# Kernel optimization log

Measured on AMD Instinct MI355X. Metric: run time of the kernel, lower is better.

## Reference

```python
import jax, jax.numpy as jnp
import numpy as np

L = 4          # n_layers
A = 4          # aspect heads: causal, intentional, temporal, normative
D = 1024       # d_model
DK = D // A    # 256
S = 3072
NE, NA = 1536, 1024  # n_events, n_agents (norms = S - NE - NA)
EPS = 1e-5


def _layernorm(x, g, b):
    mu = jnp.mean(x, axis=-1, keepdims=True)
    var = jnp.mean(jnp.square(x - mu), axis=-1, keepdims=True)
    return g * (x - mu) * jax.lax.rsqrt(var + EPS) + b


def setup_inputs() -> dict:
    key = jax.random.key(0)
    ks = jax.random.split(key, 12)
    s = 0.02
    return {
        "hidden": jax.random.normal(ks[0], (1, S, D), jnp.float32),
        "Wq": jax.random.normal(ks[1], (L, D, D), jnp.float32) * s,
        "bq": jnp.zeros((L, D), jnp.float32),
        "Wk": jax.random.normal(ks[2], (L, D, D), jnp.float32) * s,
        "bk": jnp.zeros((L, D), jnp.float32),
        "Wv": jax.random.normal(ks[3], (L, D, D), jnp.float32) * s,
        "bv": jnp.zeros((L, D), jnp.float32),
        "Wh": jax.random.normal(ks[4], (L, A, D, DK), jnp.float32) * s,
        "bh": jnp.zeros((L, A, DK), jnp.float32),
        "Wo": jax.random.normal(ks[5], (L, D, D), jnp.float32) * s,
        "bo": jnp.zeros((L, D), jnp.float32),
        "g1": jnp.ones((L, D), jnp.float32),
        "b1n": jnp.zeros((L, D), jnp.float32),
        "g2": jnp.ones((L, D), jnp.float32),
        "b2n": jnp.zeros((L, D), jnp.float32),
        "Wf1": jax.random.normal(ks[6], (L, D, 2 * D), jnp.float32) * s,
        "bf1": jnp.zeros((L, 2 * D), jnp.float32),
        "Wf2": jax.random.normal(ks[7], (L, 2 * D, D), jnp.float32) * s,
        "bf2": jnp.zeros((L, D), jnp.float32),
        "Whead": jax.random.normal(ks[8], (4, D), jnp.float32) * s,  # guilt, causation, intention, harm
        "bhead": jnp.zeros((4,), jnp.float32),
        "n_events": NE,
        "n_agents": NA,
    }


def reference(hidden, Wq, bq, Wk, bk, Wv, bv, Wh, bh, Wo, bo,
              g1, b1n, g2, b2n, Wf1, bf1, Wf2, bf2, Whead, bhead,
              n_events, n_agents):
    scale = 1.0 / np.sqrt(DK).astype(np.float32)
    h = hidden  # [B, S, D]
    for l in range(L):
        Q = h @ Wq[l] + bq[l]
        K = h @ Wk[l] + bk[l]
        V = h @ Wv[l] + bv[l]
        # per-aspect projections: [B, A, S, DK]
        Qh = jnp.einsum('bsd,ade->base', Q, Wh[l]) + bh[l][None, :, None, :]
        Kh = jnp.einsum('bsd,ade->base', K, Wh[l]) + bh[l][None, :, None, :]
        Vh = jnp.einsum('bsd,ade->base', V, Wh[l]) + bh[l][None, :, None, :]
        scores = jnp.einsum('base,bate->bast', Qh, Kh) * scale  # [B, A, S, S]
        attn = jax.nn.softmax(scores, axis=-1)  # dropout = identity (eval)
        ctx = jnp.einsum('bast,bate->base', attn, Vh)  # [B, A, S, DK]
        B = ctx.shape[0]
        ctx = ctx.transpose(0, 2, 1, 3).reshape(B, S, D)  # concat aspect heads
        attn_out = ctx @ Wo[l] + bo[l]
        h = _layernorm(h + attn_out, g1[l], b1n[l])
        ffn = jax.nn.relu(h @ Wf1[l] + bf1[l]) @ Wf2[l] + bf2[l]
        h = _layernorm(h + ffn, g2[l], b2n[l])
    event_h = h[:, :n_events, :]
    agent_h = h[:, n_events:n_events + n_agents, :]
    guilt = agent_h @ Whead[0] + bhead[0]      # [B, n_agents]
    causation = agent_h @ Whead[1] + bhead[1]
    intention = agent_h @ Whead[2] + bhead[2]
    harm = event_h @ Whead[3] + bhead[3]       # [B, n_events]
    return jnp.concatenate([guilt, causation, intention, harm], axis=-1)
```

## Files before the change

### kernel.cpp

```cpp
#include <hip/hip_runtime.h>
#include <cstdint>

typedef unsigned short u16;
typedef __bf16  bf16x8 __attribute__((ext_vector_type(8)));
typedef float   f32x4  __attribute__((ext_vector_type(4)));
typedef unsigned short u16x4 __attribute__((ext_vector_type(4)));
typedef unsigned short u16x8 __attribute__((ext_vector_type(8)));

#define S_LEN 3072
#define DMODEL 1024

__device__ __forceinline__ float bf2f(u16 u){ return __uint_as_float(((unsigned)u) << 16); }
__device__ __forceinline__ u16 f2bf(float f){
    unsigned u = __float_as_uint(f);
    return (u16)((u + 0x7fffu + ((u >> 16) & 1u)) >> 16);
}
__device__ __forceinline__ u16 cvld(const void* p, long i, int mode){
    return mode ? f2bf(((const float*)p)[i]) : ((const u16*)p)[i];
}

__device__ __forceinline__ void async16(const void* g, void* l){
    __builtin_amdgcn_global_load_lds(
        (const __attribute__((address_space(1))) unsigned int*)g,
        (__attribute__((address_space(3))) unsigned int*)l, 16, 0, 0);
}

__global__ void sniff_kernel(const u16* __restrict__ x, int* __restrict__ flag)
{
    __shared__ int r[256];
    int tid = threadIdx.x, w = 0;
    for (int j = tid; j < 4096; j += 256){
        int e = (x[j] >> 7) & 0xFF;
        if (e < 90 || e > 140) w++;
    }
    r[tid] = w; __syncthreads();
    for (int s = 128; s > 0; s >>= 1){ if (tid < s) r[tid] += r[tid + s]; __syncthreads(); }
    if (tid == 0){ flag[0] = (r[0] > 256) ? 1 : 0; flag[1] = 0; }
}


#define PSTR 72
__global__ __launch_bounds__(256)
void fused_attn(const u16* __restrict__ qkvh, u16* __restrict__ ctx)
{
    __shared__ __align__(16) u16 smem[35328];
    u16*  Kd  = smem;
    u16*  Vd  = smem + 16384;
    u16*  Pb  = smem + 32768;
    float* rsb = (float*)(smem + 32768 + 32 * PSTR);

    const int tid  = threadIdx.x;
    const int lane = tid & 63, wid = tid >> 6;
    const int quad = lane >> 4, lr = lane & 15;
    const int jx = lr & 7;
    const int h = blockIdx.y;
    const int qbase = blockIdx.x * 32;

    const u16* Q  = qkvh + (long)qbase * DMODEL + h * 256;
    const u16* K  = qkvh + (long)S_LEN * DMODEL + h * 256;
    const u16* Vt = qkvh + (long)2 * S_LEN * DMODEL + (long)h * 256 * S_LEN;

    bf16x8 qf[2][8];
#pragma unroll
    for (int mt = 0; mt < 2; ++mt)
#pragma unroll
        for (int ks = 0; ks < 8; ++ks)
            qf[mt][ks] = *(const bf16x8*)(Q + (long)(mt*16 + lr) * DMODEL + (ks*4 + quad) * 8);

    f32x4 zero = {0.f, 0.f, 0.f, 0.f};
    f32x4 oa[2][4];
#pragma unroll
    for (int mt = 0; mt < 2; ++mt)
#pragma unroll
        for (int nt = 0; nt < 4; ++nt) oa[mt][nt] = zero;
    float rsp[2][4] = {{0.f,0.f,0.f,0.f},{0.f,0.f,0.f,0.f}};

    const u16* kP[8]; const u16* vP[8]; int dOf[8];
#pragma unroll
    for (int i = 0; i < 8; ++i){
        int u = i * 256 + tid;
        int kr = u >> 5, kc = u & 31;
        kP[i] = K + (long)kr * DMODEL + (kc ^ (kr & 7)) * 8;
        int vr = u >> 3, vc = u & 7;
        vP[i] = Vt + (long)vr * S_LEN + (vc ^ (vr & 7)) * 8;
        dOf[i] = u * 8;
    }

    auto stageKV = [&](int it){
        const int kv0 = it << 6;
#pragma unroll
        for (int i = 0; i < 8; ++i) async16(kP[i] + (long)kv0 * DMODEL, Kd + dOf[i]);
#pragma unroll
        for (int i = 0; i < 8; ++i) async16(vP[i] + kv0, Vd + dOf[i]);
    };

    const float scale = 0.0625f;
    for (int it = 0; it < 48; ++it){
        __syncthreads();
        stageKV(it);
        __syncthreads();
        f32x4 sa0 = zero, sa1 = zero;
#pragma unroll
        for (int ks = 0; ks < 8; ++ks){
            const int j = (ks*4 + quad) ^ jx;
            bf16x8 kb = *(const bf16x8*)(Kd + (wid*16 + lr) * 256 + j*8);
            sa0 = __builtin_amdgcn_mfma_f32_16x16x32_bf16(qf[0][ks], kb, sa0, 0, 0, 0);
            sa1 = __builtin_amdgcn_mfma_f32_16x16x32_bf16(qf[1][ks], kb, sa1, 0, 0, 0);
        }
#pragma unroll
        for (int mt = 0; mt < 2; ++mt){
#pragma unroll
            for (int r = 0; r < 4; ++r){
                float e = __expf((mt ? sa1[r] : sa0[r]) * scale);
                rsp[mt][r] += e;
                int m = mt*16 + quad*4 + r;
                Pb[m*PSTR + (((wid*2 + (lr >> 3)) ^ (m & 7)) * 8) + (lr & 7)] = f2bf(e);
            }
        }
        __syncthreads();
#pragma unroll
        for (int ks = 0; ks < 2; ++ks){
            const int j = (ks*4 + quad) ^ jx;
            bf16x8 pa0 = *(const bf16x8*)(Pb + lr*PSTR        + j*8);
            bf16x8 pa1 = *(const bf16x8*)(Pb + (16 + lr)*PSTR + j*8);
#pragma unroll
            for (int nt = 0; nt < 4; ++nt){
                bf16x8 vb = *(const bf16x8*)(Vd + (wid*64 + nt*16 + lr) * 64 + j*8);
                oa[0][nt] = __builtin_amdgcn_mfma_f32_16x16x32_bf16(pa0, vb, oa[0][nt], 0, 0, 0);
                oa[1][nt] = __builtin_amdgcn_mfma_f32_16x16x32_bf16(pa1, vb, oa[1][nt], 0, 0, 0);
            }
        }
    }

#pragma unroll
    for (int mt = 0; mt < 2; ++mt)
#pragma unroll
        for (int r = 0; r < 4; ++r){
            float v = rsp[mt][r];
            v += __shfl_xor(v, 1, 64);
            v += __shfl_xor(v, 2, 64);
            v += __shfl_xor(v, 4, 64);
            v += __shfl_xor(v, 8, 64);
            if (lr == 0) rsb[wid*32 + mt*16 + quad*4 + r] = v;
        }
    __syncthreads();
    float inv[2][4];
#pragma unroll
    for (int mt = 0; mt < 2; ++mt)
#pragma unroll
        for (int r = 0; r < 4; ++r){
            int m = mt*16 + quad*4 + r;
            inv[mt][r] = 1.f / (rsb[m] + rsb[32 + m] + rsb[64 + m] + rsb[96 + m]);
        }
    __syncthreads();

    u16* scw = smem + (size_t)wid * (16 * 72);
    const int row_l = lane >> 2, cq = lane & 3;
#pragma unroll
    for (int mt = 0; mt < 2; ++mt){
#pragma unroll
        for (int nt = 0; nt < 4; ++nt)
#pragma unroll
            for (int r = 0; r < 4; ++r)
                scw[(quad*4 + r) * 72 + nt*16 + lr] = f2bf(oa[mt][nt][r] * inv[mt][r]);
        u16x8 p0 = *(const u16x8*)(scw + row_l * 72 + cq * 16);
        u16x8 p1 = *(const u16x8*)(scw + row_l * 72 + cq * 16 + 8);
        u16* cp = ctx + (long)(qbase + mt*16 + row_l) * DMODEL + h * 256 + wid * 64 + cq * 16;
        *(u16x8*)cp       = p0;
        *(u16x8*)(cp + 8) = p1;
    }
}

template<int SPLIT, int MODE>
__global__ __launch_bounds__(256)
void gemm128(const u16* __restrict__ A, int lda,
             const u16* __restrict__ B, int ldb,
             void* __restrict__ Cv, int ldc,
             const u16* __restrict__ bias,
             int K, long aBS, long bBS, long cBS, long pStride,
             const float* __restrict__ rs)
{
    __shared__ __align__(16) u16 smem[4 * 128 * 64];
    u16* As0 = smem;
    u16* Bs0 = smem + 2 * 128 * 64;
    const int tid  = threadIdx.x;
    const int lane = tid & 63, wid = tid >> 6;
    const int wm = wid >> 1, wn = wid & 1;
    const int quad = lane >> 4, lr = lane & 15;
    const int jx = lr & 7;

    const int z   = blockIdx.z;
    const int bat = z / SPLIT;
    const int sp  = z % SPLIT;
    const int kLen = K / SPLIT;

    A += (long)bat * aBS + (long)blockIdx.x * 128 * lda + (long)sp * kLen;
    B += (long)bat * bBS + (long)blockIdx.y * 128 * ldb + (long)sp * kLen;

    f32x4 zero = {0.f, 0.f, 0.f, 0.f};
    f32x4 acc[4][4];
#pragma unroll
    for (int i = 0; i < 4; i++)
#pragma unroll
        for (int j = 0; j < 4; j++) acc[i][j] = zero;

    const u16* aP[4]; const u16* bP[4]; int ldst[4];
#pragma unroll
    for (int i = 0; i < 4; i++){
        int u = i * 256 + tid;
        int m = u >> 3, c = u & 7;
        int cs = c ^ (m & 7);
        aP[i] = A + (long)m * lda + cs * 8;
        bP[i] = B + (long)m * ldb + cs * 8;
        ldst[i] = u * 8;
    }

    auto stage = [&](int kt, int b){
        const int k0 = kt << 6;
        u16* Ad = As0 + b * (128 * 64);
        u16* Bd = Bs0 + b * (128 * 64);
#pragma unroll
        for (int i = 0; i < 4; i++) async16(aP[i] + k0, Ad + ldst[i]);
#pragma unroll
        for (int i = 0; i < 4; i++) async16(bP[i] + k0, Bd + ldst[i]);
    };

    const int kTiles = kLen >> 6;
    stage(0, 0);
    __syncthreads();
    for (int kt = 0; kt < kTiles; ++kt){
        const int cur = kt & 1;
        if (kt + 1 < kTiles) stage(kt + 1, cur ^ 1);
        const u16* Ac = As0 + cur * (128 * 64);
        const u16* Bc = Bs0 + cur * (128 * 64);
#pragma unroll
        for (int ks = 0; ks < 2; ++ks){
            const int j = (ks * 4 + quad) ^ jx;
            bf16x8 af[4], bfg[4];
#pragma unroll
            for (int t = 0; t < 4; t++){
                int m  = wm * 64 + t * 16 + lr;
                af[t]  = *(const bf16x8*)(Ac + (m * 8 + j) * 8);
                int n  = wn * 64 + t * 16 + lr;
                bfg[t] = *(const bf16x8*)(Bc + (n * 8 + j) * 8);
            }
#pragma unroll
            for (int mt = 0; mt < 4; mt++)
#pragma unroll
                for (int nt = 0; nt < 4; nt++)
                    acc[mt][nt] = __builtin_amdgcn_mfma_f32_16x16x32_bf16(
                        af[mt], bfg[nt], acc[mt][nt], 0, 0, 0);
        }
        __syncthreads();
    }

    const int rowBase = blockIdx.x * 128 + wm * 64;
    const int colBase = blockIdx.y * 128 + wn * 64;
    const int slabw = colBase >> 10;

    if (MODE == 1 && slabw == 2){
        u16* scw = smem + (size_t)wid * (16 * 72);
        const int e_l = lane >> 2, sh = lane & 3;
#pragma unroll
        for (int nt = 0; nt < 4; nt++){
            float bv2 = bf2f(bias[colBase + nt * 16 + lr]);
#pragma unroll
            for (int mt = 0; mt < 4; mt++){
                u16x4 pk;
#pragma unroll
                for (int r = 0; r < 4; r++) pk[r] = f2bf(acc[mt][nt][r] + bv2);
                *(u16x4*)(scw + lr * 72 + mt * 16 + quad * 4) = pk;
            }
            const int e_g = (colBase & 1023) + nt * 16 + e_l;
            u16* dst = (u16*)Cv + (long)2 * S_LEN * DMODEL + (long)e_g * S_LEN
                     + rowBase + sh * 16;
            *(u16x8*)(dst)     = *(const u16x8*)(scw + e_l * 72 + sh * 16);
            *(u16x8*)(dst + 8) = *(const u16x8*)(scw + e_l * 72 + sh * 16 + 8);
        }
        return;
    }

    float* scw = (float*)smem + (size_t)wid * (16 * 68);
    const int row_l = lane >> 2, cq = lane & 3;
#pragma unroll
    for (int mt = 0; mt < 4; ++mt){
#pragma unroll
        for (int nt = 0; nt < 4; nt++)
#pragma unroll
            for (int r = 0; r < 4; r++)
                scw[(quad * 4 + r) * 68 + nt * 16 + lr] = acc[mt][nt][r];
        float vals[16];
#pragma unroll
        for (int j = 0; j < 4; j++)
            *(f32x4*)(vals + j * 4) = *(const f32x4*)(scw + row_l * 68 + cq * 16 + j * 4);
        const int row_g = rowBase + mt * 16 + row_l;
        const int colg  = colBase + cq * 16;
        float bv[16];
        if (SPLIT == 1 && bias){
            u16x8 b0 = *(const u16x8*)(bias + colg);
            u16x8 b1 = *(const u16x8*)(bias + colg + 8);
#pragma unroll
            for (int i = 0; i < 8; i++){ bv[i] = bf2f(b0[i]); bv[8 + i] = bf2f(b1[i]); }
        } else {
#pragma unroll
            for (int i = 0; i < 16; i++) bv[i] = 0.f;
        }
        u16x8 pk0, pk1;
#pragma unroll
        for (int i = 0; i < 16; i++){
            float v = vals[i] + bv[i];
            if (MODE == 2) v = fmaxf(v, 0.f);
            if (i < 8) pk0[i] = f2bf(v); else pk1[i - 8] = f2bf(v);
        }
        long idx;
        if (SPLIT > 1)      idx = (long)sp * pStride + (long)bat * cBS + (long)row_g * ldc + colg;
        else if (MODE == 1) idx = ((long)slabw * S_LEN + row_g) * DMODEL + (colg & 1023);
        else                idx = (long)bat * cBS + (long)row_g * ldc + colg;
        u16* cp = (u16*)Cv + idx;
        *(u16x8*)cp       = pk0;
        *(u16x8*)(cp + 8) = pk1;
    }
}

__global__ __launch_bounds__(256)
void wprep(const int* __restrict__ flag, int l,
           const void* Wo, const void* Wf1, const void* Wf2, const void* Wh,
           const void* Wq, const void* Wk, const void* Wv,
           u16* __restrict__ WoT, u16* __restrict__ Wf1T,
           u16* __restrict__ Wf2T, u16* __restrict__ WhT,
           u16* __restrict__ Wcat, float* __restrict__ rowSums)
{
    const int mode = *flag;
    const int z = blockIdx.x;
    const int tx = threadIdx.x, ty = threadIdx.y;

    if (z >= 7680){
        int idx = (z - 7680) * 256 + ty * 32 + tx;
        rowSums[idx] = 0.f;
        return;
    }
    if (z >= 6144){
        int t = ty * 32 + tx;
        long base = (long)(z - 6144) * 2048;
#pragma unroll
        for (int j = 0; j < 8; j++){
            long g = base + j * 256 + t;
            int slab = (int)(g >> 20);
            long r = g & 1048575;
            const void* src = (slab == 0) ? Wq : (slab == 1) ? Wk : Wv;
            Wcat[g] = cvld(src, (long)l * 1048576 + r, mode);
        }
        return;
    }

    const void* in; u16* out; long ib; int R, C, rb, cb;
    if (z < 1024){
        in = Wo; out = WoT; ib = (long)l * 1048576; R = 1024; C = 1024;
        cb = z & 31; rb = z >> 5;
    } else if (z < 3072){
        int t = z - 1024;
        in = Wf1; out = Wf1T; ib = (long)l * 2097152; R = 1024; C = 2048;
        cb = t & 63; rb = t >> 6;
    } else if (z < 5120){
        int t = z - 3072;
        in = Wf2; out = Wf2T; ib = (long)l * 2097152; R = 2048; C = 1024;
        cb = t & 31; rb = t >> 5;
    } else {
        int t = z - 5120;
        int a = t >> 8, u = t & 255;
        in = Wh; out = WhT + (long)a * 262144;
        ib = (long)l * 1048576 + (long)a * 262144; R = 1024; C = 256;
        cb = u & 7; rb = u >> 3;
    }

    __shared__ u16 tbuf[32][34];
    int r0 = rb * 32, c0 = cb * 32;
#pragma unroll
    for (int j = 0; j < 4; j++){
        int r = r0 + ty + j * 8;
        tbuf[ty + j * 8][tx] = cvld(in, ib + (long)r * C + c0 + tx, mode);
    }
    __syncthreads();
#pragma unroll
    for (int j = 0; j < 4; j++){
        int c = c0 + ty + j * 8;
        out[(long)c * R + r0 + tx] = tbuf[tx][ty + j * 8];
    }
}

__global__ __launch_bounds__(256)
void init_h(const int* __restrict__ flag, const void* __restrict__ hin,
            float* __restrict__ h, u16* __restrict__ hbf)
{
    const int mode = *flag;
    long i = (long)blockIdx.x * 256 + threadIdx.x;
    u16 u = cvld(hin, i, mode);
    h[i]   = bf2f(u);
    hbf[i] = u;
}

#define OFF_BQKV 0
#define OFF_BH   12288
#define OFF_BO   16384
#define OFF_BF1  20480
#define OFF_BF2  28672
#define OFF_G1   32768
#define OFF_B1N  36864
#define OFF_G2   40960
#define OFF_B2N  45056
#define OFF_WHD  49152
#define OFF_BHD  53248
#define BIAS_TOT 53252

__global__ __launch_bounds__(256)
void cvt_biases(const int* __restrict__ flag,
                const void* bq, const void* bk, const void* bv, const void* bh,
                const void* bo, const void* bf1, const void* bf2,
                const void* g1, const void* b1n, const void* g2, const void* b2n,
                const void* whd, const void* bhd, u16* __restrict__ A)
{
    int i = blockIdx.x * 256 + threadIdx.x;
    if (i >= BIAS_TOT) return;
    const int mode = *flag;
    u16 v;
    if (i < OFF_BH){
        int l = i / 3072, r = i % 3072;
        const void* p = (r < 1024) ? bq : (r < 2048) ? bk : bv;
        v = cvld(p, (long)l * 1024 + (r & 1023), mode);
    }
    else if (i < OFF_BO)  v = cvld(bh,  i - OFF_BH, mode);
    else if (i < OFF_BF1) v = cvld(bo,  i - OFF_BO, mode);
    else if (i < OFF_BF2) v = cvld(bf1, i - OFF_BF1, mode);
    else if (i < OFF_G1)  v = cvld(bf2, i - OFF_BF2, mode);
    else if (i < OFF_B1N) v = cvld(g1,  i - OFF_G1, mode);
    else if (i < OFF_G2)  v = cvld(b1n, i - OFF_B1N, mode);
    else if (i < OFF_B2N) v = cvld(g2,  i - OFF_G2, mode);
    else if (i < OFF_WHD) v = cvld(b2n, i - OFF_B2N, mode);
    else if (i < OFF_BHD) v = cvld(whd, i - OFF_WHD, mode);
    else                  v = cvld(bhd, i - OFF_BHD, mode);
    A[i] = v;
}

__global__ __launch_bounds__(256)
void bias_combine(const u16* __restrict__ arena, const u16* __restrict__ WhT,
                  int l, u16* __restrict__ bqkvh)
{
    int i = blockIdx.x * 256 + threadIdx.x;
    int z = i >> 10, n = i & 1023;
    const u16* bz = arena + OFF_BQKV + l * 3072 + z * 1024;
    const u16* wr = WhT + (long)n * 1024;
    float s = bf2f(arena[OFF_BH + l * 1024 + n]);
    for (int d = 0; d < 1024; d += 8){
        bf16x8 w = *(const bf16x8*)(wr + d);
        bf16x8 b = *(const bf16x8*)(bz + d);
#pragma unroll
        for (int j = 0; j < 8; j++) s += (float)w[j] * (float)b[j];
    }
    bqkvh[i] = f2bf(s);
}

__device__ __forceinline__ float blockSum(float v, float* red){
    int lane = threadIdx.x & 63, wid = threadIdx.x >> 6;
#pragma unroll
    for (int o = 32; o > 0; o >>= 1) v += __shfl_down(v, o, 64);
    __syncthreads();
    if (lane == 0) red[wid] = v;
    __syncthreads();
    return red[0] + red[1] + red[2] + red[3];
}

__global__ __launch_bounds__(256)
void ln_fused(float* __restrict__ h, const u16* __restrict__ parts, long pStride,
              int nparts, const u16* __restrict__ bias, u16* __restrict__ hbf,
              const u16* __restrict__ g, const u16* __restrict__ b)
{
    __shared__ float red[4];
    long base = (long)blockIdx.x * DMODEL;
    int tid = threadIdx.x;
    float v[4];
    float s = 0.f;
#pragma unroll
    for (int j = 0; j < 4; j++){
        int c = tid + j * 256;
        float x = bf2f(bias[c]);
        for (int sp = 0; sp < nparts; sp++) x += bf2f(parts[(long)sp * pStride + base + c]);
        float r = h[base + c] + x;
        v[j] = r; s += r;
    }
    float mu = blockSum(s, red) * (1.f / DMODEL);
    float s2 = 0.f;
#pragma unroll
    for (int j = 0; j < 4; j++){ float d = v[j] - mu; s2 += d * d; }
    float var = blockSum(s2, red) * (1.f / DMODEL);
    float inv = rsqrtf(var + 1e-5f);
#pragma unroll
    for (int j = 0; j < 4; j++){
        int c = tid + j * 256;
        float y = (v[j] - mu) * inv * bf2f(g[c]) + bf2f(b[c]);
        h[base + c]   = y;
        hbf[base + c] = f2bf(y);
    }
}

__global__ __launch_bounds__(256)
void head_kernel(const int* __restrict__ flag, const float* __restrict__ h,
                 const u16* __restrict__ arena, const int* __restrict__ nePtr,
                 const int* __restrict__ naPtr, void* __restrict__ outp)
{
    __shared__ float red[4];
    int o = blockIdx.x;
    int ne = *nePtr, na = *naPtr;
    int widx, row;
    if (o < 3 * na){ widx = o / na; row = ne + o % na; }
    else           { widx = 3;      row = o - 3 * na; }
    int tid = threadIdx.x;
    const float* hr = h + (long)row * DMODEL;
    const u16*   w  = arena + OFF_WHD + widx * DMODEL;
    float s = 0.f;
#pragma unroll
    for (int j = 0; j < 4; j++){ int c = tid + j * 256; s += hr[c] * bf2f(w[c]); }
    s = blockSum(s, red);
    if (tid == 0){
        float r = s + bf2f(arena[OFF_BHD + widx]);
        if (*flag) ((float*)outp)[o] = r;
        else       ((u16*)outp)[o]   = f2bf(r);
    }
}

extern "C" void kernel_launch(void* const* d_in, const int* in_sizes, int n_in,
                              void* d_out, int out_size, void* d_ws, size_t ws_size,
                              hipStream_t stream)
{
    const void* hidden = d_in[0];
    const void* Wq  = d_in[1];  const void* bq  = d_in[2];
    const void* Wk  = d_in[3];  const void* bk  = d_in[4];
    const void* Wv  = d_in[5];  const void* bv  = d_in[6];
    const void* Wh  = d_in[7];  const void* bh  = d_in[8];
    const void* Wo  = d_in[9];  const void* bo  = d_in[10];
    const void* g1  = d_in[11]; const void* b1n = d_in[12];
    const void* g2  = d_in[13]; const void* b2n = d_in[14];
    const void* Wf1 = d_in[15]; const void* bf1 = d_in[16];
    const void* Wf2 = d_in[17]; const void* bf2 = d_in[18];
    const void* Whd = d_in[19]; const void* bhd = d_in[20];
    const int* nePtr = (const int*)d_in[21];
    const int* naPtr = (const int*)d_in[22];

    const long D = 1024, S = 3072, L = 4;

    char* ws = (char*)d_ws;
    size_t off = 0;
    auto alloc = [&](size_t bytes)->char*{
        char* p = ws + off;
        off = (off + bytes + 255) & ~(size_t)255;
        return p;
    };
    int*  flag   = (int*)alloc(256);
    u16*  barena = (u16*)alloc(BIAS_TOT * 2);
    u16*  bqkvh  = (u16*)alloc(3 * D * 2);
    float* rowSums = (float*)alloc(4 * S * 4);
    u16*  WhT    = (u16*)alloc(D * D * 2);
    u16*  WqkvhT = (u16*)alloc(3 * D * D * 2);
    u16*  WoT    = (u16*)alloc(D * D * 2);
    u16*  Wf1T   = (u16*)alloc(2 * D * D * 2);
    u16*  Wf2T   = (u16*)alloc(2 * D * D * 2);
    float* h     = (float*)alloc(S * D * 4);
    u16*  hbf    = (u16*)alloc(S * D * 2);
    u16*  qkvh   = (u16*)alloc(3 * S * D * 2);
    u16*  ctx    = (u16*)alloc(S * D * 2);

    char* regionB = alloc((size_t)S * 2 * D * 2 + 2 * (size_t)S * D * 2);
    u16* Wcat    = (u16*)regionB;
    u16* woParts = (u16*)regionB;
    u16* ffn1    = (u16*)regionB;
    u16* f2Parts = (u16*)(regionB + (size_t)S * 2 * D * 2);

    const long pSD = S * D;

    dim3 tb(32, 8);
    sniff_kernel<<<1, 256, 0, stream>>>((const u16*)hidden, flag);
    cvt_biases<<<(BIAS_TOT + 255) / 256, 256, 0, stream>>>(
        flag, bq, bk, bv, bh, bo, bf1, bf2, g1, b1n, g2, b2n, Whd, bhd, barena);
    init_h<<<(int)(S * D / 256), 256, 0, stream>>>(flag, hidden, h, hbf);

    for (int l = 0; l < L; ++l){
        wprep<<<7728, tb, 0, stream>>>(flag, l, Wo, Wf1, Wf2, Wh, Wq, Wk, Wv,
                                       WoT, Wf1T, Wf2T, WhT, Wcat, rowSums);
        gemm128<1, 0><<<dim3(8, 8, 3), 256, 0, stream>>>(
            WhT, 1024, Wcat, 1024, WqkvhT, 1024, nullptr,
            1024, 0, (long)D * D, (long)D * D, 0, nullptr);
        bias_combine<<<12, 256, 0, stream>>>(barena, WhT, l, bqkvh);

        gemm128<1, 1><<<dim3(24, 24, 1), 256, 0, stream>>>(
            hbf, 1024, WqkvhT, 1024, qkvh, 0, bqkvh,
            1024, 0, 0, 0, 0, nullptr);

        fused_attn<<<dim3(96, 4), 256, 0, stream>>>(qkvh, ctx);

        gemm128<2, 0><<<dim3(24, 8, 2), 256, 0, stream>>>(
            ctx, 1024, WoT, 1024, woParts, 1024, nullptr,
            1024, 0, 0, 0, pSD, nullptr);
        ln_fused<<<3072, 256, 0, stream>>>(h, woParts, pSD, 2, barena + OFF_BO + l * D,
                                           hbf, barena + OFF_G1 + l * D, barena + OFF_B1N + l * D);
        gemm128<1, 2><<<dim3(24, 16, 1), 256, 0, stream>>>(
            hbf, 1024, Wf1T, 1024, ffn1, 2048, barena + OFF_BF1 + l * 2 * D,
            1024, 0, 0, 0, 0, nullptr);
        gemm128<2, 0><<<dim3(24, 8, 2), 256, 0, stream>>>(
            ffn1, 2048, Wf2T, 2048, f2Parts, 1024, nullptr,
            2048, 0, 0, 0, pSD, nullptr);
        ln_fused<<<3072, 256, 0, stream>>>(h, f2Parts, pSD, 2, barena + OFF_BF2 + l * D,
                                           hbf, barena + OFF_G2 + l * D, barena + OFF_B2N + l * D);
    }
    head_kernel<<<out_size, 256, 0, stream>>>(flag, h, barena, nePtr, naPtr, d_out);
}
```

Before: 1.251 ms.

## Register-prefetch next KV tile in fused attention and add row-normalize GEMM mode

Replaces the async global-to-LDS copy of K/V tiles with a register double-buffer: the next tile is loaded into registers while the current one is computed, then written to LDS behind a raw barrier. It also drops the padded P-buffer stride (72 to 64, still XOR-swizzled) and sets launch bounds to two blocks per SM. A new GEMM epilogue mode divides each output row by a stored row sum. That mode does not appear to be called in the visible code, so it may belong to a larger unshown change. The register prefetch raises register pressure, and the unpadded stride may add LDS bank conflicts.

```diff
diff --git a/kernel.cpp b/kernel.cpp
--- a/kernel.cpp
+++ b/kernel.cpp
@@ -39,15 +39,14 @@
 }
 
 
-#define PSTR 72
-__global__ __launch_bounds__(256)
+__global__ __launch_bounds__(256, 2)
 void fused_attn(const u16* __restrict__ qkvh, u16* __restrict__ ctx)
 {
-    __shared__ __align__(16) u16 smem[35328];
+    __shared__ __align__(16) u16 smem[35072];
     u16*  Kd  = smem;
     u16*  Vd  = smem + 16384;
     u16*  Pb  = smem + 32768;
-    float* rsb = (float*)(smem + 32768 + 32 * PSTR);
+    float* rsb = (float*)(smem + 34816);
 
     const int tid  = threadIdx.x;
     const int lane = tid & 63, wid = tid >> 6;
@@ -86,19 +85,26 @@
         dOf[i] = u * 8;
     }
 
-    auto stageKV = [&](int it){
-        const int kv0 = it << 6;
-#pragma unroll
-        for (int i = 0; i < 8; ++i) async16(kP[i] + (long)kv0 * DMODEL, Kd + dOf[i]);
-#pragma unroll
-        for (int i = 0; i < 8; ++i) async16(vP[i] + kv0, Vd + dOf[i]);
+    u16x8 kreg[8], vreg[8];
+    auto loadKV = [&](int it){
+        const long kv0 = (long)(it << 6);
+#pragma unroll
+        for (int i = 0; i < 8; ++i) kreg[i] = *(const u16x8*)(kP[i] + kv0 * DMODEL);
+#pragma unroll
+        for (int i = 0; i < 8; ++i) vreg[i] = *(const u16x8*)(vP[i] + kv0);
     };
 
     const float scale = 0.0625f;
+    loadKV(0);
     for (int it = 0; it < 48; ++it){
-        __syncthreads();
-        stageKV(it);
-        __syncthreads();
+        __builtin_amdgcn_s_barrier();
+#pragma unroll
+        for (int i = 0; i < 8; ++i) *(u16x8*)(Kd + dOf[i]) = kreg[i];
+#pragma unroll
+        for (int i = 0; i < 8; ++i) *(u16x8*)(Vd + dOf[i]) = vreg[i];
+        if (it + 1 < 48) loadKV(it + 1);
+        asm volatile("s_waitcnt lgkmcnt(0)" ::: "memory");
+        __builtin_amdgcn_s_barrier();
         f32x4 sa0 = zero, sa1 = zero;
 #pragma unroll
         for (int ks = 0; ks < 8; ++ks){
@@ -114,15 +120,16 @@
                 float e = __expf((mt ? sa1[r] : sa0[r]) * scale);
                 rsp[mt][r] += e;
                 int m = mt*16 + quad*4 + r;
-                Pb[m*PSTR + (((wid*2 + (lr >> 3)) ^ (m & 7)) * 8) + (lr & 7)] = f2bf(e);
+                Pb[m*64 + (((wid*2 + (lr >> 3)) ^ (m & 7)) * 8) + (lr & 7)] = f2bf(e);
             }
         }
-        __syncthreads();
+        asm volatile("s_waitcnt lgkmcnt(0)" ::: "memory");
+        __builtin_amdgcn_s_barrier();
 #pragma unroll
         for (int ks = 0; ks < 2; ++ks){
             const int j = (ks*4 + quad) ^ jx;
-            bf16x8 pa0 = *(const bf16x8*)(Pb + lr*PSTR        + j*8);
-            bf16x8 pa1 = *(const bf16x8*)(Pb + (16 + lr)*PSTR + j*8);
+            bf16x8 pa0 = *(const bf16x8*)(Pb + lr*64        + j*8);
+            bf16x8 pa1 = *(const bf16x8*)(Pb + (16 + lr)*64 + j*8);
 #pragma unroll
             for (int nt = 0; nt < 4; ++nt){
                 bf16x8 vb = *(const bf16x8*)(Vd + (wid*64 + nt*16 + lr) * 64 + j*8);
@@ -295,8 +302,10 @@
             *(f32x4*)(vals + j * 4) = *(const f32x4*)(scw + row_l * 68 + cq * 16 + j * 4);
         const int row_g = rowBase + mt * 16 + row_l;
         const int colg  = colBase + cq * 16;
+        float inv = 1.f;
+        if (MODE == 3) inv = 1.f / rs[(long)bat * S_LEN + row_g];
         float bv[16];
-        if (SPLIT == 1 && bias){
+        if (SPLIT == 1 && MODE != 3 && bias){
             u16x8 b0 = *(const u16x8*)(bias + colg);
             u16x8 b1 = *(const u16x8*)(bias + colg + 8);
 #pragma unroll
@@ -310,6 +319,7 @@
         for (int i = 0; i < 16; i++){
             float v = vals[i] + bv[i];
             if (MODE == 2) v = fmaxf(v, 0.f);
+            if (MODE == 3) v *= inv;
             if (i < 8) pk0[i] = f2bf(v); else pk1[i - 8] = f2bf(v);
         }
         long idx;
```

Result: slower. 1.315 ms (+5.2%).
